# Optimization experiments

Measured on AMD Instinct MI355X. Metric: run time of the kernel, lower is better.

The kernel has to match this reference:

```python
import jax, jax.numpy as jnp
import numpy as np
from jax import lax

PLENS = [2, 3, 4, 5, 6, 7]
NPAT = 50  # patterns per length
V, WD, T, H, C = 100000, 300, 2048, 100, 2
D = sum(p * 2 * NPAT for p in PLENS)  # 2700 diag rows actually used


def setup_inputs() -> dict:
    key = jax.random.key(0)
    ks = jax.random.split(key, 20)
    inp = {}
    inp['doc'] = jax.random.randint(ks[0], (T,), 0, V)
    inp['embeddings'] = jax.random.normal(ks[1], (V, WD), jnp.float32)
    diags = jax.random.normal(ks[2], (D, WD), jnp.float32)
    diags = diags / jnp.linalg.norm(diags, axis=1, keepdims=True)  # normalize() in __init__
    inp['diags'] = diags
    inp['bias'] = jax.random.normal(ks[3], (D,), jnp.float32)
    for i, p in enumerate(PLENS):
        inp[f'eps{p}'] = jax.random.normal(ks[4 + i], (NPAT, p - 1), jnp.float32)
    inp['epsilon_scale'] = 0.5 * jnp.ones((1,), jnp.float32)
    inp['self_loop_scale'] = 0.5 * jnp.ones((1,), jnp.float32)
    tot = NPAT * len(PLENS)  # 300
    inp['w1'] = jax.random.normal(ks[10], (tot, H), jnp.float32) * 0.05
    inp['b1'] = jax.random.normal(ks[11], (H,), jnp.float32) * 0.05
    inp['w2'] = jax.random.normal(ks[12], (H, C), jnp.float32) * 0.05
    inp['b2'] = jax.random.normal(ks[13], (C,), jnp.float32) * 0.05
    return inp


def _run_group(tm, eps, sls, plen):
    # tm: [T, NPAT, 2, plen]; eps: [NPAT, plen-1]; sls: [1] (self-loop scale)
    # sum-times semiring: zero=0, one=1, plus=add, times=mul
    one_col = jnp.ones((NPAT, 1), tm.dtype)
    zero_col = jnp.zeros((NPAT, 1), tm.dtype)
    h0 = jnp.concatenate([one_col, jnp.zeros((NPAT, plen - 1), tm.dtype)], axis=1)

    def step(carry, tm_t):
        h, sc = carry
        # epsilon transitions
        h = h + jnp.concatenate([zero_col, h[:, :-1] * eps], axis=1)
        # main (word) transitions with restart padding (semiring one)
        res = jnp.concatenate([one_col, h[:, :-1] * tm_t[:, 1, :-1]], axis=1)
        # scaled self-loops
        res = res + sls * (h * tm_t[:, 0, :])
        return (res, sc + res[:, -1]), None

    (_, sc), _ = lax.scan(step, (h0, jnp.zeros((NPAT,), tm.dtype)), tm)
    return sc  # [NPAT]


def reference(doc, embeddings, diags, bias, eps2, eps3, eps4, eps5, eps6, eps7,
              epsilon_scale, self_loop_scale, w1, b1, w2, b2):
    # all per-token transition values at once: [T, D]
    tm_full = jax.nn.sigmoid(embeddings[doc] @ diags.T + bias)
    sls = jax.nn.sigmoid(self_loop_scale)
    eps_sc = jax.nn.sigmoid(epsilon_scale)
    eps_list = [eps2, eps3, eps4, eps5, eps6, eps7]
    scores = []
    start = 0
    for p, eps_raw in zip(PLENS, eps_list):
        end = start + p * 2 * NPAT
        tm = tm_full[:, start:end].reshape(-1, NPAT, 2, p)
        eps = eps_sc * jax.nn.sigmoid(eps_raw)
        scores.append(_run_group(tm, eps, sls, p))
        start = end
    s = jnp.concatenate(scores)[None, :]  # [1, total_num_patterns]
    h = jax.nn.relu(s @ w1 + b1)
    return h @ w2 + b2  # logits [1, num_classes]
```

## Files before the change

### kernel.cpp

```cpp
#include <hip/hip_runtime.h>
#include <math.h>

#define T_LEN 2048
#define WD 300
#define DTOT 2700
#define NPAT 50
#define NGROUP 6
#define H_DIM 100
#define NCLS 2
#define CCH 64
#define SCH 32
#define TOTPAT 300
#define RSTRIDE 68

__device__ __forceinline__ float sigm(float x) { return 1.f / (1.f + __expf(-x)); }

__global__ __launch_bounds__(256) void gather_kernel(const int* __restrict__ doc,
                                                     const float* __restrict__ emb,
                                                     float* __restrict__ Edoc) {
    int gid = blockIdx.x * 256 + threadIdx.x;
    int t = gid / 75;
    int q = gid - t * 75;
    int tok = doc[t];
    *(float4*)(Edoc + (size_t)t * WD + q * 4) =
        *(const float4*)(emb + (size_t)tok * WD + q * 4);
}

#define BM 128
#define BN 64
#define BK 32

__global__ __launch_bounds__(256) void gemm_sig(const float* __restrict__ A,
                                                const float* __restrict__ Bm,
                                                const float* __restrict__ bias,
                                                float* __restrict__ Cm) {
    __shared__ alignas(16) float As[BK][BM];
    __shared__ alignas(16) float Bs[BK][BN];
    int tid = threadIdx.x;
    int tx = tid & 15;
    int ty = tid >> 4;
    int m0 = blockIdx.y * BM;
    int n0 = blockIdx.x * BN;

    float acc[8][4];
#pragma unroll
    for (int i = 0; i < 8; ++i)
#pragma unroll
        for (int j = 0; j < 4; ++j) acc[i][j] = 0.f;

    for (int k0 = 0; k0 < WD; k0 += BK) {
#pragma unroll
        for (int it = 0; it < 4; ++it) {
            int f = (it << 8) + tid;
            int row = f >> 3;
            int kq = f & 7;
            int k = k0 + (kq << 2);
            float4 av = make_float4(0.f, 0.f, 0.f, 0.f);
            if (k < WD) av = *(const float4*)(A + (size_t)(m0 + row) * WD + k);
            int kk = kq << 2;
            As[kk + 0][row] = av.x;
            As[kk + 1][row] = av.y;
            As[kk + 2][row] = av.z;
            As[kk + 3][row] = av.w;
        }
#pragma unroll
        for (int it = 0; it < 2; ++it) {
            int f = (it << 8) + tid;
            int row = f >> 3;
            int kq = f & 7;
            int k = k0 + (kq << 2);
            int nr = n0 + row;
            if (nr > DTOT - 1) nr = DTOT - 1;
            float4 bv = make_float4(0.f, 0.f, 0.f, 0.f);
            if (k < WD) bv = *(const float4*)(Bm + (size_t)nr * WD + k);
            int kk = kq << 2;
            Bs[kk + 0][row] = bv.x;
            Bs[kk + 1][row] = bv.y;
            Bs[kk + 2][row] = bv.z;
            Bs[kk + 3][row] = bv.w;
        }
        __syncthreads();
#pragma unroll
        for (int kk = 0; kk < BK; ++kk) {
            float4 a0 = *(const float4*)&As[kk][ty * 8];
            float4 a1 = *(const float4*)&As[kk][ty * 8 + 4];
            float4 b0 = *(const float4*)&Bs[kk][tx * 4];
            float aa[8] = {a0.x, a0.y, a0.z, a0.w, a1.x, a1.y, a1.z, a1.w};
            float bb[4] = {b0.x, b0.y, b0.z, b0.w};
#pragma unroll
            for (int i = 0; i < 8; ++i)
#pragma unroll
                for (int j = 0; j < 4; ++j) acc[i][j] = fmaf(aa[i], bb[j], acc[i][j]);
        }
        __syncthreads();
    }

    int n = n0 + (tx << 2);
    if (n + 3 < DTOT) {
        float4 bsv = *(const float4*)(bias + n);
#pragma unroll
        for (int i = 0; i < 8; ++i) {
            int m = m0 + ty * 8 + i;
            float4 o;
            o.x = sigm(acc[i][0] + bsv.x);
            o.y = sigm(acc[i][1] + bsv.y);
            o.z = sigm(acc[i][2] + bsv.z);
            o.w = sigm(acc[i][3] + bsv.w);
            *(float4*)(Cm + (size_t)m * DTOT + n) = o;
        }
    }
}

template <int P>
__device__ void pass1_group(int idx, const float* __restrict__ tm,
                            const float* __restrict__ epsr,
                            float sls, float esc, float* __restrict__ ws2, int g) {
    constexpr int NP1 = P + 1;
    int chunk = idx / (NPAT * NP1);
    int rem = idx - chunk * (NPAT * NP1);
    int pat = rem / NP1;
    int col = rem - pat * NP1;
    const int dstart = 100 * ((P * (P - 1)) / 2 - 1);

    float eps[P > 1 ? P - 1 : 1];
#pragma unroll
    for (int j = 0; j < P - 1; ++j) eps[j] = esc * sigm(epsr[pat * (P - 1) + j]);

    float x[P];
#pragma unroll
    for (int i = 0; i < P; ++i) x[i] = 0.f;
    float inj = 0.f;
    if (col < P) x[col] = 1.f; else inj = 1.f;
    float qacc = 0.f;

    const float* tp = tm + (size_t)(chunk * SCH) * DTOT + dstart + pat * 2 * P;
#pragma unroll 4
    for (int t = 0; t < SCH; ++t) {
        float cs[P], cw[P > 1 ? P - 1 : 1];
#pragma unroll
        for (int i = 0; i < P; ++i) cs[i] = tp[i];
#pragma unroll
        for (int i = 0; i < P - 1; ++i) cw[i] = tp[P + i];
        tp += DTOT;

        float heps[P];
        heps[0] = x[0];
#pragma unroll
        for (int i = 1; i < P; ++i) heps[i] = fmaf(x[i - 1], eps[i - 1], x[i]);
        float res[P];
        res[0] = fmaf(heps[0], sls * cs[0], inj);
#pragma unroll
        for (int i = 1; i < P; ++i)
            res[i] = fmaf(heps[i - 1], cw[i - 1], heps[i] * (sls * cs[i]));
#pragma unroll
        for (int i = 0; i < P; ++i) x[i] = res[i];
        qacc += x[P - 1];
    }

    int gidx = g * NPAT + pat;
    float* dst = ws2 + ((size_t)(gidx * CCH + chunk)) * 64 + col * 8;
#pragma unroll
    for (int i = 0; i < P; ++i) dst[i] = x[i];
    dst[7] = qacc;
}

__global__ __launch_bounds__(64) void pass1_kernel(const float* __restrict__ tm,
                                                   const float* __restrict__ e2,
                                                   const float* __restrict__ e3,
                                                   const float* __restrict__ e4,
                                                   const float* __restrict__ e5,
                                                   const float* __restrict__ e6,
                                                   const float* __restrict__ e7,
                                                   const float* __restrict__ eps_scale,
                                                   const float* __restrict__ sl_scale,
                                                   float* __restrict__ ws2) {
    int tid = blockIdx.x * 64 + threadIdx.x;
    float sls = sigm(sl_scale[0]);
    float esc = sigm(eps_scale[0]);
    if (tid < 9600)        pass1_group<2>(tid,          tm, e2, sls, esc, ws2, 0);
    else if (tid < 22400)  pass1_group<3>(tid - 9600,   tm, e3, sls, esc, ws2, 1);
    else if (tid < 38400)  pass1_group<4>(tid - 22400,  tm, e4, sls, esc, ws2, 2);
    else if (tid < 57600)  pass1_group<5>(tid - 38400,  tm, e5, sls, esc, ws2, 3);
    else if (tid < 80000)  pass1_group<6>(tid - 57600,  tm, e6, sls, esc, ws2, 4);
    else                   pass1_group<7>(tid - 80000,  tm, e7, sls, esc, ws2, 5);
}

template <int P>
__device__ __forceinline__ void compose_rec(float* __restrict__ Arec,
                                            const float* __restrict__ Brec) {
    float MA[P][P], MB[P][P], vA[P], vB[P], qA[P], qB[P], rA, rB;
#pragma unroll
    for (int j = 0; j < P; ++j) {
#pragma unroll
        for (int i = 0; i < P; ++i) {
            MA[i][j] = Arec[j * 8 + i];
            MB[i][j] = Brec[j * 8 + i];
        }
        qA[j] = Arec[j * 8 + 7];
        qB[j] = Brec[j * 8 + 7];
    }
#pragma unroll
    for (int i = 0; i < P; ++i) {
        vA[i] = Arec[P * 8 + i];
        vB[i] = Brec[P * 8 + i];
    }
    rA = Arec[P * 8 + 7];
    rB = Brec[P * 8 + 7];

#pragma unroll
    for (int j = 0; j < P; ++j) {
        float mc[P];
#pragma unroll
        for (int i = 0; i < P; ++i) mc[i] = 0.f;
        float qc = qA[j];
#pragma unroll
        for (int k = 0; k < P; ++k) {
            float a = MA[k][j];
#pragma unroll
            for (int i = 0; i < P; ++i) mc[i] = fmaf(MB[i][k], a, mc[i]);
            qc = fmaf(qB[k], a, qc);
        }
#pragma unroll
        for (int i = 0; i < P; ++i) Arec[j * 8 + i] = mc[i];
        Arec[j * 8 + 7] = qc;
    }
    float vc[P];
#pragma unroll
    for (int i = 0; i < P; ++i) vc[i] = vB[i];
    float rc = rA + rB;
#pragma unroll
    for (int k = 0; k < P; ++k) {
        float a = vA[k];
#pragma unroll
        for (int i = 0; i < P; ++i) vc[i] = fmaf(MB[i][k], a, vc[i]);
        rc = fmaf(qB[k], a, rc);
    }
#pragma unroll
    for (int i = 0; i < P; ++i) Arec[P * 8 + i] = vc[i];
    Arec[P * 8 + 7] = rc;
}

template <int P>
__device__ void fold_pattern(const float* __restrict__ ws2, float* __restrict__ R,
                             float* __restrict__ scores, int gidx, int tid) {
    const float4* src = (const float4*)(ws2 + (size_t)gidx * CCH * 64);
#pragma unroll
    for (int j = 0; j < 16; ++j) {
        int f = j * 64 + tid;
        int rec = f >> 4;
        int q4 = f & 15;
        *(float4*)&R[rec * RSTRIDE + q4 * 4] = src[f];
    }
    for (int g = 1; g < CCH; g <<= 1) {
        __syncthreads();
        if ((tid & (2 * g - 1)) == 0)
            compose_rec<P>(&R[tid * RSTRIDE], &R[(tid + g) * RSTRIDE]);
    }
    __syncthreads();
    if (tid == 0) scores[gidx] = R[0 * 8 + 7] + R[P * 8 + 7];
}

__global__ __launch_bounds__(64) void pass2a_kernel(const float* __restrict__ ws2,
                                                    float* __restrict__ scores) {
    __shared__ float R[CCH * RSTRIDE];
    int gidx = blockIdx.x;
    int g = gidx / NPAT;
    int tid = threadIdx.x;
    switch (g) {
        case 0: fold_pattern<2>(ws2, R, scores, gidx, tid); break;
        case 1: fold_pattern<3>(ws2, R, scores, gidx, tid); break;
        case 2: fold_pattern<4>(ws2, R, scores, gidx, tid); break;
        case 3: fold_pattern<5>(ws2, R, scores, gidx, tid); break;
        case 4: fold_pattern<6>(ws2, R, scores, gidx, tid); break;
        case 5: fold_pattern<7>(ws2, R, scores, gidx, tid); break;
    }
}

__global__ __launch_bounds__(128) void mlp_kernel(const float* __restrict__ scores,
                                                  const float* __restrict__ w1,
                                                  const float* __restrict__ b1,
                                                  const float* __restrict__ w2,
                                                  const float* __restrict__ b2,
                                                  float* __restrict__ out) {
    __shared__ float s_lds[TOTPAT];
    __shared__ float h_lds[H_DIM];
    int tid = threadIdx.x;
    for (int i = tid; i < TOTPAT; i += 128) s_lds[i] = scores[i];
    __syncthreads();
    if (tid < H_DIM) {
        float a = b1[tid];
#pragma unroll 6
        for (int i = 0; i < TOTPAT; ++i) a = fmaf(s_lds[i], w1[i * H_DIM + tid], a);
        h_lds[tid] = fmaxf(a, 0.f);
    }
    __syncthreads();
    if (tid < NCLS) {
        float a = b2[tid];
        for (int j = 0; j < H_DIM; ++j) a = fmaf(h_lds[j], w2[j * NCLS + tid], a);
        out[tid] = a;
    }
}

extern "C" void kernel_launch(void* const* d_in, const int* in_sizes, int n_in,
                              void* d_out, int out_size, void* d_ws, size_t ws_size,
                              hipStream_t stream) {
    const int* doc = (const int*)d_in[0];
    const float* emb = (const float*)d_in[1];
    const float* diags = (const float*)d_in[2];
    const float* bias = (const float*)d_in[3];
    const float* e2 = (const float*)d_in[4];
    const float* e3 = (const float*)d_in[5];
    const float* e4 = (const float*)d_in[6];
    const float* e5 = (const float*)d_in[7];
    const float* e6 = (const float*)d_in[8];
    const float* e7 = (const float*)d_in[9];
    const float* eps_scale = (const float*)d_in[10];
    const float* sl_scale = (const float*)d_in[11];
    const float* w1 = (const float*)d_in[12];
    const float* b1 = (const float*)d_in[13];
    const float* w2 = (const float*)d_in[14];
    const float* b2 = (const float*)d_in[15];
    float* out = (float*)d_out;

    char* ws = (char*)d_ws;
    float* Edoc = (float*)ws;
    float* tm = (float*)(ws + 2457600);
    float* ws2 = (float*)(ws + 2457600 + 22118400);
    float* scores = Edoc;

    hipLaunchKernelGGL(gather_kernel, dim3((T_LEN * 75) / 256), dim3(256), 0, stream,
                       doc, emb, Edoc);
    hipLaunchKernelGGL(gemm_sig, dim3((DTOT + BN - 1) / BN, T_LEN / BM), dim3(256), 0,
                       stream, Edoc, diags, bias, tm);
    hipLaunchKernelGGL(pass1_kernel, dim3(105600 / 64), dim3(64), 0, stream,
                       tm, e2, e3, e4, e5, e6, e7, eps_scale, sl_scale, ws2);
    hipLaunchKernelGGL(pass2a_kernel, dim3(TOTPAT), dim3(64), 0, stream,
                       ws2, scores);
    hipLaunchKernelGGL(mlp_kernel, dim3(1), dim3(128), 0, stream,
                       scores, w1, b1, w2, b2, out);
}
```

Before: 292.0 us.

## Use split-bf16 MFMA GEMM and LDS-staged tiles for pass1 scan

Replaces the FP32 SIMT GEMM with a prepack step that splits the embeddings and diagonals into high and low bf16 halves, then runs a bf16 MFMA GEMM using three products to keep close to fp32 accuracy. Pass1 now stages each pattern block's transition values for a time chunk into shared memory with coalesced float4 loads, instead of each thread reading strided global memory directly. The aim is to use matrix cores for the projection and to coalesce the scan's loads. The cost is an extra prepack pass, some loss of precision, and workspace regions that ws2 and Ah now share.

```diff
diff --git a/kernel.cpp b/kernel.cpp
--- a/kernel.cpp
+++ b/kernel.cpp
@@ -5,163 +5,217 @@
 #define WD 300
 #define DTOT 2700
 #define NPAT 50
-#define NGROUP 6
 #define H_DIM 100
 #define NCLS 2
 #define CCH 64
 #define SCH 32
 #define TOTPAT 300
 #define RSTRIDE 68
+#define KP 320
+#define ASTR 40
+
+typedef short bf16x8 __attribute__((ext_vector_type(8)));
+typedef float f32x4 __attribute__((ext_vector_type(4)));
 
 __device__ __forceinline__ float sigm(float x) { return 1.f / (1.f + __expf(-x)); }
 
-__global__ __launch_bounds__(256) void gather_kernel(const int* __restrict__ doc,
-                                                     const float* __restrict__ emb,
-                                                     float* __restrict__ Edoc) {
+__device__ __forceinline__ unsigned short f2bf(float x) {
+    unsigned int u = __float_as_uint(x);
+    u += 0x7fffu + ((u >> 16) & 1u);
+    return (unsigned short)(u >> 16);
+}
+__device__ __forceinline__ float bf2f(unsigned short h) {
+    return __uint_as_float(((unsigned int)h) << 16);
+}
+
+#define NA2 (T_LEN * (KP / 2))
+#define NB2 (DTOT * (KP / 2))
+
+__global__ __launch_bounds__(256) void prepack(const int* __restrict__ doc,
+                                               const float* __restrict__ emb,
+                                               const float* __restrict__ diags,
+                                               unsigned short* __restrict__ Ah,
+                                               unsigned short* __restrict__ Al,
+                                               unsigned short* __restrict__ Bh,
+                                               unsigned short* __restrict__ Bl) {
     int gid = blockIdx.x * 256 + threadIdx.x;
-    int t = gid / 75;
-    int q = gid - t * 75;
-    int tok = doc[t];
-    *(float4*)(Edoc + (size_t)t * WD + q * 4) =
-        *(const float4*)(emb + (size_t)tok * WD + q * 4);
-}
-
-#define BM 128
-#define BN 64
-#define BK 32
-
-__global__ __launch_bounds__(256) void gemm_sig(const float* __restrict__ A,
-                                                const float* __restrict__ Bm,
-                                                const float* __restrict__ bias,
-                                                float* __restrict__ Cm) {
-    __shared__ alignas(16) float As[BK][BM];
-    __shared__ alignas(16) float Bs[BK][BN];
+    float2 v = make_float2(0.f, 0.f);
+    unsigned short* ph;
+    unsigned short* pl;
+    size_t off;
+    if (gid < NA2) {
+        int t = gid / (KP / 2);
+        int kk = (gid - t * (KP / 2)) * 2;
+        if (kk < WD) v = *(const float2*)(emb + (size_t)doc[t] * WD + kk);
+        off = (size_t)t * KP + kk;
+        ph = Ah; pl = Al;
+    } else {
+        int b = gid - NA2;
+        if (b >= NB2) return;
+        int n = b / (KP / 2);
+        int kk = (b - n * (KP / 2)) * 2;
+        if (kk < WD) v = *(const float2*)(diags + (size_t)n * WD + kk);
+        off = (size_t)n * KP + kk;
+        ph = Bh; pl = Bl;
+    }
+    unsigned short h0 = f2bf(v.x), h1 = f2bf(v.y);
+    unsigned short l0 = f2bf(v.x - bf2f(h0)), l1 = f2bf(v.y - bf2f(h1));
+    ushort2 hv; hv.x = h0; hv.y = h1;
+    ushort2 lv; lv.x = l0; lv.y = l1;
+    *(ushort2*)(ph + off) = hv;
+    *(ushort2*)(pl + off) = lv;
+}
+
+__global__ __launch_bounds__(256) void gemm_mfma(const unsigned short* __restrict__ Ah,
+                                                 const unsigned short* __restrict__ Al,
+                                                 const unsigned short* __restrict__ Bh,
+                                                 const unsigned short* __restrict__ Bl,
+                                                 const float* __restrict__ bias,
+                                                 float* __restrict__ Cm) {
+    __shared__ unsigned short sA[2][128][ASTR];
+    __shared__ unsigned short sB[2][64][ASTR];
     int tid = threadIdx.x;
-    int tx = tid & 15;
-    int ty = tid >> 4;
-    int m0 = blockIdx.y * BM;
-    int n0 = blockIdx.x * BN;
-
-    float acc[8][4];
-#pragma unroll
-    for (int i = 0; i < 8; ++i)
-#pragma unroll
-        for (int j = 0; j < 4; ++j) acc[i][j] = 0.f;
-
-    for (int k0 = 0; k0 < WD; k0 += BK) {
-#pragma unroll
-        for (int it = 0; it < 4; ++it) {
-            int f = (it << 8) + tid;
-            int row = f >> 3;
-            int kq = f & 7;
-            int k = k0 + (kq << 2);
-            float4 av = make_float4(0.f, 0.f, 0.f, 0.f);
-            if (k < WD) av = *(const float4*)(A + (size_t)(m0 + row) * WD + k);
-            int kk = kq << 2;
-            As[kk + 0][row] = av.x;
-            As[kk + 1][row] = av.y;
-            As[kk + 2][row] = av.z;
-            As[kk + 3][row] = av.w;
-        }
+    int lane = tid & 63, wid = tid >> 6;
+    int m0 = blockIdx.y * 128, n0 = blockIdx.x * 64;
+    int wm = (wid >> 1) * 64;
+    int wn = (wid & 1) * 32;
+
+    f32x4 acc[4][2];
+#pragma unroll
+    for (int mi = 0; mi < 4; ++mi)
+#pragma unroll
+        for (int ni = 0; ni < 2; ++ni) acc[mi][ni] = (f32x4)(0.f);
+
+    for (int k0 = 0; k0 < KP; k0 += 32) {
 #pragma unroll
         for (int it = 0; it < 2; ++it) {
-            int f = (it << 8) + tid;
-            int row = f >> 3;
-            int kq = f & 7;
-            int k = k0 + (kq << 2);
-            int nr = n0 + row;
-            if (nr > DTOT - 1) nr = DTOT - 1;
-            float4 bv = make_float4(0.f, 0.f, 0.f, 0.f);
-            if (k < WD) bv = *(const float4*)(Bm + (size_t)nr * WD + k);
-            int kk = kq << 2;
-            Bs[kk + 0][row] = bv.x;
-            Bs[kk + 1][row] = bv.y;
-            Bs[kk + 2][row] = bv.z;
-            Bs[kk + 3][row] = bv.w;
+            int f = it * 256 + tid;
+            int row = f >> 2, q = f & 3;
+            size_t go = (size_t)(m0 + row) * KP + k0 + q * 8;
+            *(uint4*)&sA[0][row][q * 8] = *(const uint4*)(Ah + go);
+            *(uint4*)&sA[1][row][q * 8] = *(const uint4*)(Al + go);
+        }
+        {
+            int row = tid >> 2, q = tid & 3;
+            int nr = n0 + row; if (nr > DTOT - 1) nr = DTOT - 1;
+            size_t go = (size_t)nr * KP + k0 + q * 8;
+            *(uint4*)&sB[0][row][q * 8] = *(const uint4*)(Bh + go);
+            *(uint4*)&sB[1][row][q * 8] = *(const uint4*)(Bl + go);
         }
         __syncthreads();
-#pragma unroll
-        for (int kk = 0; kk < BK; ++kk) {
-            float4 a0 = *(const float4*)&As[kk][ty * 8];
-            float4 a1 = *(const float4*)&As[kk][ty * 8 + 4];
-            float4 b0 = *(const float4*)&Bs[kk][tx * 4];
-            float aa[8] = {a0.x, a0.y, a0.z, a0.w, a1.x, a1.y, a1.z, a1.w};
-            float bb[4] = {b0.x, b0.y, b0.z, b0.w};
-#pragma unroll
-            for (int i = 0; i < 8; ++i)
-#pragma unroll
-                for (int j = 0; j < 4; ++j) acc[i][j] = fmaf(aa[i], bb[j], acc[i][j]);
-        }
+
+        int kc = (lane >> 4) * 8;
+        int mr = lane & 15;
+        bf16x8 ah[4], al[4], bh[2], bl[2];
+#pragma unroll
+        for (int mi = 0; mi < 4; ++mi) {
+            ah[mi] = *(bf16x8*)&sA[0][wm + mi * 16 + mr][kc];
+            al[mi] = *(bf16x8*)&sA[1][wm + mi * 16 + mr][kc];
+        }
+#pragma unroll
+        for (int ni = 0; ni < 2; ++ni) {
+            bh[ni] = *(bf16x8*)&sB[0][wn + ni * 16 + mr][kc];
+            bl[ni] = *(bf16x8*)&sB[1][wn + ni * 16 + mr][kc];
+        }
+#pragma unroll
+        for (int mi = 0; mi < 4; ++mi)
+#pragma unroll
+            for (int ni = 0; ni < 2; ++ni) {
+                acc[mi][ni] = __builtin_amdgcn_mfma_f32_16x16x32_bf16(ah[mi], bh[ni], acc[mi][ni], 0, 0, 0);
+                acc[mi][ni] = __builtin_amdgcn_mfma_f32_16x16x32_bf16(ah[mi], bl[ni], acc[mi][ni], 0, 0, 0);
+                acc[mi][ni] = __builtin_amdgcn_mfma_f32_16x16x32_bf16(al[mi], bh[ni], acc[mi][ni], 0, 0, 0);
+            }
         __syncthreads();
     }
 
-    int n = n0 + (tx << 2);
-    if (n + 3 < DTOT) {
-        float4 bsv = *(const float4*)(bias + n);
-#pragma unroll
-        for (int i = 0; i < 8; ++i) {
-            int m = m0 + ty * 8 + i;
-            float4 o;
-            o.x = sigm(acc[i][0] + bsv.x);
-            o.y = sigm(acc[i][1] + bsv.y);
-            o.z = sigm(acc[i][2] + bsv.z);
-            o.w = sigm(acc[i][3] + bsv.w);
-            *(float4*)(Cm + (size_t)m * DTOT + n) = o;
-        }
-    }
-}
-
-template <int P>
-__device__ void pass1_group(int idx, const float* __restrict__ tm,
-                            const float* __restrict__ epsr,
-                            float sls, float esc, float* __restrict__ ws2, int g) {
+    int mr = lane & 15;
+    int rq = lane >> 4;
+#pragma unroll
+    for (int ni = 0; ni < 2; ++ni) {
+        int col = n0 + wn + ni * 16 + mr;
+        int cc = col < DTOT ? col : DTOT - 1;
+        float bs = bias[cc];
+        if (col < DTOT) {
+#pragma unroll
+            for (int mi = 0; mi < 4; ++mi)
+#pragma unroll
+                for (int r = 0; r < 4; ++r) {
+                    int row = m0 + wm + mi * 16 + rq * 4 + r;
+                    Cm[(size_t)row * DTOT + col] = sigm(acc[mi][ni][r] + bs);
+                }
+        }
+    }
+}
+
+template <int P, int PBP>
+__device__ void pass1_blk(int chunk, int patblk, const float* __restrict__ tm,
+                          const float* __restrict__ epsr, float sls, float esc,
+                          float* __restrict__ ws2, int g, float* __restrict__ sT,
+                          int tid) {
     constexpr int NP1 = P + 1;
-    int chunk = idx / (NPAT * NP1);
-    int rem = idx - chunk * (NPAT * NP1);
-    int pat = rem / NP1;
-    int col = rem - pat * NP1;
-    const int dstart = 100 * ((P * (P - 1)) / 2 - 1);
-
-    float eps[P > 1 ? P - 1 : 1];
-#pragma unroll
-    for (int j = 0; j < P - 1; ++j) eps[j] = esc * sigm(epsr[pat * (P - 1) + j]);
-
-    float x[P];
-#pragma unroll
-    for (int i = 0; i < P; ++i) x[i] = 0.f;
-    float inj = 0.f;
-    if (col < P) x[col] = 1.f; else inj = 1.f;
-    float qacc = 0.f;
-
-    const float* tp = tm + (size_t)(chunk * SCH) * DTOT + dstart + pat * 2 * P;
+    constexpr int dstart = 100 * ((P * (P - 1)) / 2 - 1);
+    constexpr int ROWF = PBP * 2 * P;
+    constexpr int RB4 = ROWF / 4;
+    constexpr int NF4 = SCH * RB4;
+
+    const float* gbase = tm + (size_t)(chunk * SCH) * DTOT + dstart + patblk * ROWF;
+#pragma unroll
+    for (int i = 0; i < (NF4 + 63) / 64; ++i) {
+        int f = i * 64 + tid;
+        if (f < NF4) {
+            int t = f / RB4;
+            int q = f - t * RB4;
+            *(float4*)&sT[t * ROWF + q * 4] = *(const float4*)(gbase + (size_t)t * DTOT + q * 4);
+        }
+    }
+    __syncthreads();
+
+    int patl = tid / NP1;
+    int col = tid - patl * NP1;
+    int pat = patblk * PBP + patl;
+    if (patl < PBP && pat < NPAT) {
+        float eps[P - 1];
+#pragma unroll
+        for (int j = 0; j < P - 1; ++j) eps[j] = esc * sigm(epsr[pat * (P - 1) + j]);
+
+        float x[P];
+#pragma unroll
+        for (int i = 0; i < P; ++i) x[i] = 0.f;
+        float inj = 0.f;
+        if (col < P) x[col] = 1.f; else inj = 1.f;
+        float qacc = 0.f;
+
+        const float* lb = sT + patl * 2 * P;
 #pragma unroll 4
-    for (int t = 0; t < SCH; ++t) {
-        float cs[P], cw[P > 1 ? P - 1 : 1];
-#pragma unroll
-        for (int i = 0; i < P; ++i) cs[i] = tp[i];
-#pragma unroll
-        for (int i = 0; i < P - 1; ++i) cw[i] = tp[P + i];
-        tp += DTOT;
-
-        float heps[P];
-        heps[0] = x[0];
-#pragma unroll
-        for (int i = 1; i < P; ++i) heps[i] = fmaf(x[i - 1], eps[i - 1], x[i]);
-        float res[P];
-        res[0] = fmaf(heps[0], sls * cs[0], inj);
-#pragma unroll
-        for (int i = 1; i < P; ++i)
-            res[i] = fmaf(heps[i - 1], cw[i - 1], heps[i] * (sls * cs[i]));
-#pragma unroll
-        for (int i = 0; i < P; ++i) x[i] = res[i];
-        qacc += x[P - 1];
-    }
-
-    int gidx = g * NPAT + pat;
-    float* dst = ws2 + ((size_t)(gidx * CCH + chunk)) * 64 + col * 8;
-#pragma unroll
-    for (int i = 0; i < P; ++i) dst[i] = x[i];
-    dst[7] = qacc;
+        for (int t = 0; t < SCH; ++t) {
+            float tv[2 * P];
+            const float* row = lb + t * ROWF;
+#pragma unroll
+            for (int j = 0; j < P; ++j) {
+                float2 u = *(const float2*)(row + 2 * j);
+                tv[2 * j] = u.x;
+                tv[2 * j + 1] = u.y;
+            }
+            float heps[P];
+            heps[0] = x[0];
+#pragma unroll
+            for (int i = 1; i < P; ++i) heps[i] = fmaf(x[i - 1], eps[i - 1], x[i]);
+            float res[P];
+            res[0] = fmaf(heps[0], sls * tv[0], inj);
+#pragma unroll
+            for (int i = 1; i < P; ++i)
+                res[i] = fmaf(heps[i - 1], tv[P + i - 1], heps[i] * (sls * tv[i]));
+#pragma unroll
+            for (int i = 0; i < P; ++i) x[i] = res[i];
+            qacc += x[P - 1];
+        }
+
+        int gidx = g * NPAT + pat;
+        float* dst = ws2 + ((size_t)(gidx * CCH + chunk)) * 64 + col * 8;
+#pragma unroll
+        for (int i = 0; i < P; ++i) dst[i] = x[i];
+        dst[7] = qacc;
+    }
 }
 
 __global__ __launch_bounds__(64) void pass1_kernel(const float* __restrict__ tm,
@@ -174,15 +228,19 @@
                                                    const float* __restrict__ eps_scale,
                                                    const float* __restrict__ sl_scale,
                                                    float* __restrict__ ws2) {
-    int tid = blockIdx.x * 64 + threadIdx.x;
+    __shared__ float sT[3584];
+    int b = blockIdx.x;
+    int chunk = b / 30;
+    int r = b - chunk * 30;
+    int tid = threadIdx.x;
     float sls = sigm(sl_scale[0]);
     float esc = sigm(eps_scale[0]);
-    if (tid < 9600)        pass1_group<2>(tid,          tm, e2, sls, esc, ws2, 0);
-    else if (tid < 22400)  pass1_group<3>(tid - 9600,   tm, e3, sls, esc, ws2, 1);
-    else if (tid < 38400)  pass1_group<4>(tid - 22400,  tm, e4, sls, esc, ws2, 2);
-    else if (tid < 57600)  pass1_group<5>(tid - 38400,  tm, e5, sls, esc, ws2, 3);
-    else if (tid < 80000)  pass1_group<6>(tid - 57600,  tm, e6, sls, esc, ws2, 4);
-    else                   pass1_group<7>(tid - 80000,  tm, e7, sls, esc, ws2, 5);
+    if (r < 3)       pass1_blk<2, 21>(chunk, r,      tm, e2, sls, esc, ws2, 0, sT, tid);
+    else if (r < 7)  pass1_blk<3, 16>(chunk, r - 3,  tm, e3, sls, esc, ws2, 1, sT, tid);
+    else if (r < 12) pass1_blk<4, 12>(chunk, r - 7,  tm, e4, sls, esc, ws2, 2, sT, tid);
+    else if (r < 17) pass1_blk<5, 10>(chunk, r - 12, tm, e5, sls, esc, ws2, 3, sT, tid);
+    else if (r < 23) pass1_blk<6, 9>(chunk, r - 17,  tm, e6, sls, esc, ws2, 4, sT, tid);
+    else             pass1_blk<7, 8>(chunk, r - 23,  tm, e7, sls, esc, ws2, 5, sT, tid);
 }
 
 template <int P>
@@ -323,16 +381,19 @@
     float* out = (float*)d_out;
 
     char* ws = (char*)d_ws;
-    float* Edoc = (float*)ws;
-    float* tm = (float*)(ws + 2457600);
-    float* ws2 = (float*)(ws + 2457600 + 22118400);
-    float* scores = Edoc;
-
-    hipLaunchKernelGGL(gather_kernel, dim3((T_LEN * 75) / 256), dim3(256), 0, stream,
-                       doc, emb, Edoc);
-    hipLaunchKernelGGL(gemm_sig, dim3((DTOT + BN - 1) / BN, T_LEN / BM), dim3(256), 0,
-                       stream, Edoc, diags, bias, tm);
-    hipLaunchKernelGGL(pass1_kernel, dim3(105600 / 64), dim3(64), 0, stream,
+    float* tm = (float*)ws;
+    float* ws2 = (float*)(ws + 22118400);
+    unsigned short* Ah = (unsigned short*)(ws + 22118400);
+    unsigned short* Al = (unsigned short*)(ws + 23429120);
+    unsigned short* Bh = (unsigned short*)(ws + 24739840);
+    unsigned short* Bl = (unsigned short*)(ws + 26467840);
+    float* scores = (float*)(ws + 28195840);
+
+    hipLaunchKernelGGL(prepack, dim3((NA2 + NB2 + 255) / 256), dim3(256), 0, stream,
+                       doc, emb, diags, Ah, Al, Bh, Bl);
+    hipLaunchKernelGGL(gemm_mfma, dim3((DTOT + 63) / 64, T_LEN / 128), dim3(256), 0,
+                       stream, Ah, Al, Bh, Bl, bias, tm);
+    hipLaunchKernelGGL(pass1_kernel, dim3(CCH * 30), dim3(64), 0, stream,
                        tm, e2, e3, e4, e5, e6, e7, eps_scale, sl_scale, ws2);
     hipLaunchKernelGGL(pass2a_kernel, dim3(TOTPAT), dim3(64), 0, stream,
                        ws2, scores);
```

Result: faster. 248.9 us (-14.8%).
